# Performance work log

Measured on AMD Instinct MI355X. Metric: run time of the kernel, lower is better.

Reference implementation:

```python
import jax, jax.numpy as jnp
import numpy as np

B, C, L = 256, 500, 200
D, H, NUM_ITEMS = 64, 128, 100000
BETA = 0.7
EPS = 1e-8


def _xavier(key, fan_in, fan_out):
    lim = float(np.sqrt(6.0 / (fan_in + fan_out)))
    return jax.random.uniform(key, (fan_in, fan_out), minval=-lim, maxval=lim, dtype=jnp.float32)


def setup_inputs() -> dict:
    key = jax.random.key(0)
    ks = jax.random.split(key, 12)
    inp = {
        'candidate_items': jax.random.randint(ks[0], (B, C), 0, NUM_ITEMS, dtype=jnp.int64) if jax.config.read('jax_enable_x64') else jax.random.randint(ks[0], (B, C), 0, NUM_ITEMS),
        'query_times': jax.random.uniform(ks[1], (B,), dtype=jnp.float32),
        'candidate_histories': jax.random.uniform(ks[2], (B, C, L), dtype=jnp.float32),
        'item_emb': 0.02 * jax.random.normal(ks[3], (NUM_ITEMS, D), dtype=jnp.float32),
        'base_W1': _xavier(ks[4], D, H), 'base_b1': jnp.zeros((H,), jnp.float32),
        'base_W2': _xavier(ks[5], H, H), 'base_b2': jnp.zeros((H,), jnp.float32),
        'base_W3': _xavier(ks[6], H, 1),
        'exc_W1': _xavier(ks[7], D, H), 'exc_b1': jnp.zeros((H,), jnp.float32),
        'exc_W2': _xavier(ks[8], H, H), 'exc_b2': jnp.zeros((H,), jnp.float32),
        'exc_W3': _xavier(ks[9], H, 1),
    }
    return inp


def _mlp(x, W1, b1, W2, b2, W3):
    # (Linear + Softplus) x depth, then Linear -> 1 (no bias), squeeze last dim
    h = jax.nn.softplus(x @ W1 + b1)
    h = jax.nn.softplus(h @ W2 + b2)
    return (h @ W3)[..., 0]


def reference(candidate_items, query_times, candidate_histories, item_emb,
              base_W1, base_b1, base_W2, base_b2, base_W3,
              exc_W1, exc_b1, exc_W2, exc_b2, exc_W3):
    z = item_emb[candidate_items]                                  # [B, C, D]
    mu = jax.nn.softplus(_mlp(z, base_W1, base_b1, base_W2, base_b2, base_W3)) + EPS   # [B, C]
    alpha = jax.nn.softplus(_mlp(z, exc_W1, exc_b1, exc_W2, exc_b2, exc_W3)) + EPS     # [B, C]
    q = query_times[:, None, None]                                 # [B, 1, 1]
    mask = candidate_histories < q                                 # [B, C, L]
    delta = jnp.maximum(q - candidate_histories, 0.0)              # clamp(min=0)
    h = jnp.sum(jnp.exp(-BETA * delta) * mask, axis=-1)            # [B, C]
    return mu + alpha * h
```

## Files before the change

kernel.cpp:

```cpp
#include <hip/hip_runtime.h>
#include <math.h>

#define BB 256
#define CC 500
#define LL 200
#define DD 64
#define HH 128
#define NUM_ITEMS 100000
#define BETA 0.7f
#define EPSV 1e-8f

#define TM 32
#define WPB 4
#define NTILE (NUM_ITEMS / TM)
#define NWSET 1024
#define SETBLK (NWSET / WPB)

typedef _Float16 half8 __attribute__((ext_vector_type(8)));
typedef float floatx4 __attribute__((ext_vector_type(4)));

__device__ __forceinline__ float softplus_safe(float x) {
    float t = __expf(-fabsf(x));
    return fmaxf(x, 0.0f) + __logf(1.0f + t);
}
__device__ __forceinline__ float softplus_fast(float x) {
    return __logf(1.0f + __expf(x));
}
__device__ __forceinline__ float softplus_small(float x) {
    float z = x * x;
    float p = fmaf(fmaf(-5.2083333e-3f, z, 0.125f), z, 0.69314718f);
    return fmaf(x, 0.5f, p);
}

__global__ __launch_bounds__(256) void prep_w(
    const float* __restrict__ W1, const float* __restrict__ W2,
    const float* __restrict__ V1, const float* __restrict__ V2,
    _Float16* __restrict__ wb)
{
    int t = blockIdx.x * 256 + threadIdx.x;
    if (t >= 49152) return;
    float v;
    if (t < 8192)       { int n = t >> 6,  k = t & 63;             v = W1[k * HH + n]; }
    else if (t < 24576) { int u = t - 8192;  int n = u >> 7, k = u & 127; v = W2[k * HH + n]; }
    else if (t < 32768) { int u = t - 24576; int n = u >> 6, k = u & 63;  v = V1[k * HH + n]; }
    else                { int u = t - 32768; int n = u >> 7, k = u & 127; v = V2[k * HH + n]; }
    wb[t] = (_Float16)v;
}

__device__ __forceinline__ void prefetch_z(const float* __restrict__ emb, int t,
                                           int l15, int quad, floatx4 (&zraw)[2][2][2]) {
    #pragma unroll
    for (int mt = 0; mt < 2; ++mt) {
        const float* p = emb + (size_t)(t * TM + mt * 16 + l15) * DD + quad * 8;
        #pragma unroll
        for (int kt = 0; kt < 2; ++kt) {
            zraw[mt][kt][0] = *(const floatx4*)(p + kt * 32);
            zraw[mt][kt][1] = *(const floatx4*)(p + kt * 32 + 4);
        }
    }
}

__global__ __launch_bounds__(256, 1) void mlp_mfma(
    const float* __restrict__ emb, const _Float16* __restrict__ wb,
    const float* __restrict__ b1, const float* __restrict__ b2, const float* __restrict__ W3,
    const float* __restrict__ c1, const float* __restrict__ c2, const float* __restrict__ V3,
    float* __restrict__ mu, float* __restrict__ alpha)
{
    __shared__ __align__(16) _Float16 h1s[WPB * TM * HH];
    int tid  = threadIdx.x;
    int wave = tid >> 6, lane = tid & 63;
    int quad = lane >> 4, l15 = lane & 15;

    int is_exc = blockIdx.x >= SETBLK;
    int wslot  = (blockIdx.x - (is_exc ? SETBLK : 0)) * WPB + wave;

    const _Float16* W1t = wb + (is_exc ? 24576 : 0);
    const _Float16* W2t = wb + (is_exc ? 32768 : 8192);
    const float* B1  = is_exc ? c1 : b1;
    const float* B2  = is_exc ? c2 : b2;
    const float* W3p = is_exc ? V3 : W3;
    float* outp = is_exc ? alpha : mu;
    _Float16* hs = h1s + wave * (TM * HH);

    half8 w1f[2][2][4];
    half8 w2f[2][4][4];
    float b1v[2][4], b2v[2][4], w3v[2][4];
    #pragma unroll
    for (int h = 0; h < 2; ++h)
        #pragma unroll
        for (int n = 0; n < 4; ++n) {
            int j = (h * 4 + n) * 16 + l15;
            b1v[h][n] = B1[j];
            b2v[h][n] = B2[j];
            w3v[h][n] = W3p[j];
            #pragma unroll
            for (int kt = 0; kt < 2; ++kt)
                w1f[h][kt][n] = *(const half8*)(W1t + j * DD + kt * 32 + quad * 8);
            #pragma unroll
            for (int kt = 0; kt < 4; ++kt)
                w2f[h][kt][n] = *(const half8*)(W2t + j * HH + kt * 32 + quad * 8);
        }

    floatx4 zraw[2][2][2];
    prefetch_z(emb, wslot, l15, quad, zraw);

    #pragma unroll 1
    for (int t = wslot; t < NTILE; t += NWSET) {
        half8 zf[2][2];
        #pragma unroll
        for (int mt = 0; mt < 2; ++mt)
            #pragma unroll
            for (int kt = 0; kt < 2; ++kt) {
                half8 z;
                #pragma unroll
                for (int j = 0; j < 4; ++j) {
                    z[j]     = (_Float16)zraw[mt][kt][0][j];
                    z[4 + j] = (_Float16)zraw[mt][kt][1][j];
                }
                zf[mt][kt] = z;
            }
        int tn = (t + NWSET < NTILE) ? t + NWSET : t;
        prefetch_z(emb, tn, l15, quad, zraw);

        #pragma unroll
        for (int h = 0; h < 2; ++h) {
            floatx4 acc[2][4];
            #pragma unroll
            for (int n = 0; n < 4; ++n) {
                float bv = b1v[h][n];
                #pragma unroll
                for (int mt = 0; mt < 2; ++mt) acc[mt][n] = (floatx4){bv, bv, bv, bv};
            }
            #pragma unroll
            for (int kt = 0; kt < 2; ++kt)
                #pragma unroll
                for (int n = 0; n < 4; ++n)
                    #pragma unroll
                    for (int mt = 0; mt < 2; ++mt)
                        acc[mt][n] = __builtin_amdgcn_mfma_f32_16x16x32_f16(zf[mt][kt], w1f[h][kt][n], acc[mt][n], 0, 0, 0);
            #pragma unroll
            for (int mt = 0; mt < 2; ++mt)
                #pragma unroll
                for (int n = 0; n < 4; ++n)
                    #pragma unroll
                    for (int r = 0; r < 4; ++r) {
                        int itq = quad * 4 + r;
                        int sw  = ((h * 4 + n) * 2 + (l15 >> 3)) ^ itq;
                        hs[(mt * 16 + itq) * HH + sw * 8 + (l15 & 7)] =
                            (_Float16)softplus_small(acc[mt][n][r]);
                    }
        }

        float sacc[2][4];
        #pragma unroll
        for (int mt = 0; mt < 2; ++mt)
            #pragma unroll
            for (int r = 0; r < 4; ++r) sacc[mt][r] = 0.0f;

        #pragma unroll
        for (int h = 0; h < 2; ++h) {
            floatx4 acc[2][4];
            #pragma unroll
            for (int n = 0; n < 4; ++n) {
                float bv = b2v[h][n];
                #pragma unroll
                for (int mt = 0; mt < 2; ++mt) acc[mt][n] = (floatx4){bv, bv, bv, bv};
            }
            #pragma unroll
            for (int kt = 0; kt < 4; ++kt) {
                half8 af[2];
                #pragma unroll
                for (int mt = 0; mt < 2; ++mt)
                    af[mt] = *(const half8*)(hs + (mt * 16 + l15) * HH + (((kt * 4 + quad) ^ l15) * 8));
                #pragma unroll
                for (int n = 0; n < 4; ++n)
                    #pragma unroll
                    for (int mt = 0; mt < 2; ++mt)
                        acc[mt][n] = __builtin_amdgcn_mfma_f32_16x16x32_f16(af[mt], w2f[h][kt][n], acc[mt][n], 0, 0, 0);
            }
            #pragma unroll
            for (int n = 0; n < 4; ++n) {
                float w3 = w3v[h][n];
                #pragma unroll
                for (int mt = 0; mt < 2; ++mt)
                    #pragma unroll
                    for (int r = 0; r < 4; ++r)
                        sacc[mt][r] += softplus_fast(acc[mt][n][r]) * w3;
            }
        }
        #pragma unroll
        for (int mt = 0; mt < 2; ++mt)
            #pragma unroll
            for (int r = 0; r < 4; ++r) {
                float s = sacc[mt][r];
                s += __shfl_xor(s, 1, 64);
                s += __shfl_xor(s, 2, 64);
                s += __shfl_xor(s, 4, 64);
                s += __shfl_xor(s, 8, 64);
                if (l15 == 0)
                    outp[t * TM + mt * 16 + quad * 4 + r] = softplus_safe(s) + EPSV;
            }
    }
}

__global__ __launch_bounds__(256) void hawkes_kernel(
    const int* __restrict__ items,
    const float* __restrict__ qt,
    const float* __restrict__ hist,
    const float* __restrict__ mu,
    const float* __restrict__ alpha,
    float* __restrict__ out)
{
    int w = blockIdx.x * 4 + (threadIdx.x >> 6);
    int lane = threadIdx.x & 63;
    float q = qt[w / CC];

    float s = 0.0f;
    if (lane < LL / 4) {
        float4 v = *(const float4*)(hist + (size_t)w * LL + lane * 4);
        s  = (v.x < q) ? __expf(BETA * v.x) : 0.f;
        s += (v.y < q) ? __expf(BETA * v.y) : 0.f;
        s += (v.z < q) ? __expf(BETA * v.z) : 0.f;
        s += (v.w < q) ? __expf(BETA * v.w) : 0.f;
    }
    #pragma unroll
    for (int off = 1; off < 64; off <<= 1) s += __shfl_xor(s, off, 64);

    if (lane == 0) {
        int it = items[w];
        out[w] = fmaf(alpha[it] * __expf(-BETA * q), s, mu[it]);
    }
}

extern "C" void kernel_launch(void* const* d_in, const int* in_sizes, int n_in,
                              void* d_out, int out_size, void* d_ws, size_t ws_size,
                              hipStream_t stream)
{
    const int*   items = (const int*)  d_in[0];
    const float* qt    = (const float*)d_in[1];
    const float* hist  = (const float*)d_in[2];
    const float* emb   = (const float*)d_in[3];
    const float* W1    = (const float*)d_in[4];
    const float* b1    = (const float*)d_in[5];
    const float* W2    = (const float*)d_in[6];
    const float* b2    = (const float*)d_in[7];
    const float* W3    = (const float*)d_in[8];
    const float* V1    = (const float*)d_in[9];
    const float* c1    = (const float*)d_in[10];
    const float* V2    = (const float*)d_in[11];
    const float* c2    = (const float*)d_in[12];
    const float* V3    = (const float*)d_in[13];

    float* out = (float*)d_out;
    _Float16* wb = (_Float16*)d_ws;
    float* mu    = (float*)((char*)d_ws + 98304);
    float* alpha = mu + NUM_ITEMS;

    prep_w<<<192, 256, 0, stream>>>(W1, W2, V1, V2, wb);

    mlp_mfma<<<2 * SETBLK, WPB * 64, 0, stream>>>(emb, wb, b1, b2, W3, c1, c2, V3, mu, alpha);

    hawkes_kernel<<<(BB * CC) / 4, 256, 0, stream>>>(items, qt, hist, mu, alpha, out);
}
```

Before: 250.3 us.

## Split MLP hidden dimension across waves with shared LDS tile per block

Before, each wave computed the whole 128-wide hidden layer for its own 32-item tile. Now the four waves of a block share one 32-item tile, and each wave owns 32 hidden units. The layer-2 partial outputs are reduced across waves through LDS, with two block barriers per tile. This cuts the per-wave weight registers to a quarter so more blocks fit per CU (launch bounds raised to 4), in exchange for added synchronisation. The software prefetch of the next tile's embeddings is dropped, so the change relies on occupancy instead to hide memory latency.

```diff
diff --git a/kernel.cpp b/kernel.cpp
--- a/kernel.cpp
+++ b/kernel.cpp
@@ -13,8 +13,7 @@
 #define TM 32
 #define WPB 4
 #define NTILE (NUM_ITEMS / TM)
-#define NWSET 1024
-#define SETBLK (NWSET / WPB)
+#define BPS 1024
 
 typedef _Float16 half8 __attribute__((ext_vector_type(8)));
 typedef float floatx4 __attribute__((ext_vector_type(4)));
@@ -47,32 +46,20 @@
     wb[t] = (_Float16)v;
 }
 
-__device__ __forceinline__ void prefetch_z(const float* __restrict__ emb, int t,
-                                           int l15, int quad, floatx4 (&zraw)[2][2][2]) {
-    #pragma unroll
-    for (int mt = 0; mt < 2; ++mt) {
-        const float* p = emb + (size_t)(t * TM + mt * 16 + l15) * DD + quad * 8;
-        #pragma unroll
-        for (int kt = 0; kt < 2; ++kt) {
-            zraw[mt][kt][0] = *(const floatx4*)(p + kt * 32);
-            zraw[mt][kt][1] = *(const floatx4*)(p + kt * 32 + 4);
-        }
-    }
-}
-
-__global__ __launch_bounds__(256, 1) void mlp_mfma(
+__global__ __launch_bounds__(256, 4) void mlp_mfma(
     const float* __restrict__ emb, const _Float16* __restrict__ wb,
     const float* __restrict__ b1, const float* __restrict__ b2, const float* __restrict__ W3,
     const float* __restrict__ c1, const float* __restrict__ c2, const float* __restrict__ V3,
     float* __restrict__ mu, float* __restrict__ alpha)
 {
-    __shared__ __align__(16) _Float16 h1s[WPB * TM * HH];
+    __shared__ __align__(16) _Float16 h1s[TM * HH];
+    __shared__ __align__(16) float    part[TM * WPB];
     int tid  = threadIdx.x;
-    int wave = tid >> 6, lane = tid & 63;
+    int w    = tid >> 6, lane = tid & 63;
     int quad = lane >> 4, l15 = lane & 15;
 
-    int is_exc = blockIdx.x >= SETBLK;
-    int wslot  = (blockIdx.x - (is_exc ? SETBLK : 0)) * WPB + wave;
+    int is_exc = blockIdx.x >= BPS;
+    int bslot  = blockIdx.x - (is_exc ? BPS : 0);
 
     const _Float16* W1t = wb + (is_exc ? 24576 : 0);
     const _Float16* W2t = wb + (is_exc ? 32768 : 8192);
@@ -80,113 +67,102 @@
     const float* B2  = is_exc ? c2 : b2;
     const float* W3p = is_exc ? V3 : W3;
     float* outp = is_exc ? alpha : mu;
-    _Float16* hs = h1s + wave * (TM * HH);
-
-    half8 w1f[2][2][4];
-    half8 w2f[2][4][4];
-    float b1v[2][4], b2v[2][4], w3v[2][4];
+
+    half8 w1f[2][2];
+    half8 w2f[4][2];
+    float b1v[2], b2v[2], w3v[2];
     #pragma unroll
-    for (int h = 0; h < 2; ++h)
-        #pragma unroll
-        for (int n = 0; n < 4; ++n) {
-            int j = (h * 4 + n) * 16 + l15;
-            b1v[h][n] = B1[j];
-            b2v[h][n] = B2[j];
-            w3v[h][n] = W3p[j];
-            #pragma unroll
-            for (int kt = 0; kt < 2; ++kt)
-                w1f[h][kt][n] = *(const half8*)(W1t + j * DD + kt * 32 + quad * 8);
-            #pragma unroll
-            for (int kt = 0; kt < 4; ++kt)
-                w2f[h][kt][n] = *(const half8*)(W2t + j * HH + kt * 32 + quad * 8);
-        }
-
-    floatx4 zraw[2][2][2];
-    prefetch_z(emb, wslot, l15, quad, zraw);
+    for (int n = 0; n < 2; ++n) {
+        int j = (2 * w + n) * 16 + l15;
+        b1v[n] = B1[j];
+        b2v[n] = B2[j];
+        w3v[n] = W3p[j];
+        #pragma unroll
+        for (int kt = 0; kt < 2; ++kt)
+            w1f[kt][n] = *(const half8*)(W1t + j * DD + kt * 32 + quad * 8);
+        #pragma unroll
+        for (int kt = 0; kt < 4; ++kt)
+            w2f[kt][n] = *(const half8*)(W2t + j * HH + kt * 32 + quad * 8);
+    }
 
     #pragma unroll 1
-    for (int t = wslot; t < NTILE; t += NWSET) {
+    for (int t = bslot; t < NTILE; t += BPS) {
         half8 zf[2][2];
         #pragma unroll
-        for (int mt = 0; mt < 2; ++mt)
+        for (int mt = 0; mt < 2; ++mt) {
+            const float* p = emb + (size_t)(t * TM + mt * 16 + l15) * DD + quad * 8;
             #pragma unroll
             for (int kt = 0; kt < 2; ++kt) {
+                floatx4 v0 = *(const floatx4*)(p + kt * 32);
+                floatx4 v1 = *(const floatx4*)(p + kt * 32 + 4);
                 half8 z;
                 #pragma unroll
                 for (int j = 0; j < 4; ++j) {
-                    z[j]     = (_Float16)zraw[mt][kt][0][j];
-                    z[4 + j] = (_Float16)zraw[mt][kt][1][j];
+                    z[j] = (_Float16)v0[j]; z[4 + j] = (_Float16)v1[j];
                 }
                 zf[mt][kt] = z;
             }
-        int tn = (t + NWSET < NTILE) ? t + NWSET : t;
-        prefetch_z(emb, tn, l15, quad, zraw);
-
-        #pragma unroll
-        for (int h = 0; h < 2; ++h) {
-            floatx4 acc[2][4];
-            #pragma unroll
-            for (int n = 0; n < 4; ++n) {
-                float bv = b1v[h][n];
-                #pragma unroll
-                for (int mt = 0; mt < 2; ++mt) acc[mt][n] = (floatx4){bv, bv, bv, bv};
-            }
-            #pragma unroll
-            for (int kt = 0; kt < 2; ++kt)
-                #pragma unroll
-                for (int n = 0; n < 4; ++n)
-                    #pragma unroll
-                    for (int mt = 0; mt < 2; ++mt)
-                        acc[mt][n] = __builtin_amdgcn_mfma_f32_16x16x32_f16(zf[mt][kt], w1f[h][kt][n], acc[mt][n], 0, 0, 0);
+        }
+
+        floatx4 acc1[2][2];
+        #pragma unroll
+        for (int n = 0; n < 2; ++n) {
+            float bv = b1v[n];
+            #pragma unroll
+            for (int mt = 0; mt < 2; ++mt) acc1[mt][n] = (floatx4){bv, bv, bv, bv};
+        }
+        #pragma unroll
+        for (int kt = 0; kt < 2; ++kt)
+            #pragma unroll
+            for (int n = 0; n < 2; ++n)
+                #pragma unroll
+                for (int mt = 0; mt < 2; ++mt)
+                    acc1[mt][n] = __builtin_amdgcn_mfma_f32_16x16x32_f16(zf[mt][kt], w1f[kt][n], acc1[mt][n], 0, 0, 0);
+        #pragma unroll
+        for (int mt = 0; mt < 2; ++mt)
+            #pragma unroll
+            for (int n = 0; n < 2; ++n)
+                #pragma unroll
+                for (int r = 0; r < 4; ++r) {
+                    int itq = quad * 4 + r;
+                    int sw  = ((2 * w + n) * 2 + (l15 >> 3)) ^ itq;
+                    h1s[(mt * 16 + itq) * HH + sw * 8 + (l15 & 7)] =
+                        (_Float16)softplus_small(acc1[mt][n][r]);
+                }
+        __syncthreads();
+
+        floatx4 acc2[2][2];
+        #pragma unroll
+        for (int n = 0; n < 2; ++n) {
+            float bv = b2v[n];
+            #pragma unroll
+            for (int mt = 0; mt < 2; ++mt) acc2[mt][n] = (floatx4){bv, bv, bv, bv};
+        }
+        #pragma unroll
+        for (int kt = 0; kt < 4; ++kt) {
+            half8 af[2];
             #pragma unroll
             for (int mt = 0; mt < 2; ++mt)
-                #pragma unroll
-                for (int n = 0; n < 4; ++n)
-                    #pragma unroll
-                    for (int r = 0; r < 4; ++r) {
-                        int itq = quad * 4 + r;
-                        int sw  = ((h * 4 + n) * 2 + (l15 >> 3)) ^ itq;
-                        hs[(mt * 16 + itq) * HH + sw * 8 + (l15 & 7)] =
-                            (_Float16)softplus_small(acc[mt][n][r]);
-                    }
-        }
-
+                af[mt] = *(const half8*)(h1s + (mt * 16 + l15) * HH + (((kt * 4 + quad) ^ l15) * 8));
+            #pragma unroll
+            for (int n = 0; n < 2; ++n)
+                #pragma unroll
+                for (int mt = 0; mt < 2; ++mt)
+                    acc2[mt][n] = __builtin_amdgcn_mfma_f32_16x16x32_f16(af[mt], w2f[kt][n], acc2[mt][n], 0, 0, 0);
+        }
         float sacc[2][4];
         #pragma unroll
         for (int mt = 0; mt < 2; ++mt)
             #pragma unroll
             for (int r = 0; r < 4; ++r) sacc[mt][r] = 0.0f;
-
-        #pragma unroll
-        for (int h = 0; h < 2; ++h) {
-            floatx4 acc[2][4];
-            #pragma unroll
-            for (int n = 0; n < 4; ++n) {
-                float bv = b2v[h][n];
-                #pragma unroll
-                for (int mt = 0; mt < 2; ++mt) acc[mt][n] = (floatx4){bv, bv, bv, bv};
-            }
-            #pragma unroll
-            for (int kt = 0; kt < 4; ++kt) {
-                half8 af[2];
-                #pragma unroll
-                for (int mt = 0; mt < 2; ++mt)
-                    af[mt] = *(const half8*)(hs + (mt * 16 + l15) * HH + (((kt * 4 + quad) ^ l15) * 8));
-                #pragma unroll
-                for (int n = 0; n < 4; ++n)
-                    #pragma unroll
-                    for (int mt = 0; mt < 2; ++mt)
-                        acc[mt][n] = __builtin_amdgcn_mfma_f32_16x16x32_f16(af[mt], w2f[h][kt][n], acc[mt][n], 0, 0, 0);
-            }
-            #pragma unroll
-            for (int n = 0; n < 4; ++n) {
-                float w3 = w3v[h][n];
-                #pragma unroll
-                for (int mt = 0; mt < 2; ++mt)
-                    #pragma unroll
-                    for (int r = 0; r < 4; ++r)
-                        sacc[mt][r] += softplus_fast(acc[mt][n][r]) * w3;
-            }
+        #pragma unroll
+        for (int n = 0; n < 2; ++n) {
+            float w3 = w3v[n];
+            #pragma unroll
+            for (int mt = 0; mt < 2; ++mt)
+                #pragma unroll
+                for (int r = 0; r < 4; ++r)
+                    sacc[mt][r] += softplus_fast(acc2[mt][n][r]) * w3;
         }
         #pragma unroll
         for (int mt = 0; mt < 2; ++mt)
@@ -198,8 +174,15 @@
                 s += __shfl_xor(s, 4, 64);
                 s += __shfl_xor(s, 8, 64);
                 if (l15 == 0)
-                    outp[t * TM + mt * 16 + quad * 4 + r] = softplus_safe(s) + EPSV;
+                    part[(mt * 16 + quad * 4 + r) * WPB + w] = s;
             }
+        __syncthreads();
+
+        if (tid < TM) {
+            floatx4 pv = *(const floatx4*)(part + tid * WPB);
+            float s = (pv[0] + pv[1]) + (pv[2] + pv[3]);
+            outp[t * TM + tid] = softplus_safe(s) + EPSV;
+        }
     }
 }
 
@@ -258,7 +241,7 @@
 
     prep_w<<<192, 256, 0, stream>>>(W1, W2, V1, V2, wb);
 
-    mlp_mfma<<<2 * SETBLK, WPB * 64, 0, stream>>>(emb, wb, b1, b2, W3, c1, c2, V3, mu, alpha);
+    mlp_mfma<<<2 * BPS, WPB * 64, 0, stream>>>(emb, wb, b1, b2, W3, c1, c2, V3, mu, alpha);
 
     hawkes_kernel<<<(BB * CC) / 4, 256, 0, stream>>>(items, qt, hist, mu, alpha, out);
 }
```

After: 239.9 us. -4.1%, faster.
